# Performance work log

Measured on AMD Instinct MI355X. Metric: run time of the kernel, lower is better.

The kernel has to match this reference:

```python
import jax, jax.numpy as jnp
import numpy as np
from jax import lax

D_MODEL, D_INNER, D_STATE, D_CONV, DT_RANK = 128, 256, 16, 4, 8
BATCH, SEQ = 8, 4096


def setup_inputs() -> dict:
    key = jax.random.key(0)
    ks = jax.random.split(key, 13)
    g = lambda k, shape, fan: (jax.random.normal(k, shape, jnp.float32) / np.sqrt(fan)).astype(jnp.float32)
    inp = {
        "s": jax.random.normal(ks[0], (BATCH, SEQ, D_MODEL), jnp.float32),
        "in_proj_w": g(ks[1], (2 * D_INNER, D_MODEL), D_MODEL),
        "conv_w": g(ks[2], (D_INNER, 1, D_CONV), D_CONV),
        "conv_b": jnp.zeros((D_INNER,), jnp.float32),
        "x_proj_w": g(ks[3], (DT_RANK + 2 * D_STATE, D_INNER), D_INNER),
        "dt_proj_w": g(ks[4], (D_INNER, DT_RANK), DT_RANK),
        "dt_proj_b": jax.random.uniform(ks[5], (D_INNER,), jnp.float32, -4.0, -2.0),  # softplus(b) small, like mamba dt init
        "A_log": jnp.log(jnp.broadcast_to(jnp.arange(1, D_STATE + 1, dtype=jnp.float32), (D_INNER, D_STATE))),
        "D_skip": jnp.ones((D_INNER,), jnp.float32),
        "out_proj_w": g(ks[6], (D_MODEL, D_INNER), D_INNER),
        "ln_gamma": jnp.ones((D_MODEL,), jnp.float32),
        "ln_beta": jnp.zeros((D_MODEL,), jnp.float32),
        "fc_w": g(ks[7], (D_MODEL, D_MODEL), D_MODEL),
    }
    return inp


def _mamba(s, in_proj_w, conv_w, conv_b, x_proj_w, dt_proj_w, dt_proj_b, A_log, D_skip, out_proj_w):
    B, L, _ = s.shape
    xz = jnp.einsum("bld,ed->ble", s, in_proj_w)           # [B,L,2*D_INNER]
    x, z = jnp.split(xz, 2, axis=-1)                        # each [B,L,D_INNER]
    # causal depthwise conv1d
    xc = jnp.transpose(x, (0, 2, 1))                        # [B,D_INNER,L]
    xc = jnp.pad(xc, ((0, 0), (0, 0), (D_CONV - 1, 0)))
    xc = lax.conv_general_dilated(xc, conv_w, (1,), "VALID",
                                  dimension_numbers=("NCH", "OIH", "NCH"),
                                  feature_group_count=D_INNER)
    x = jax.nn.silu(jnp.transpose(xc + conv_b[None, :, None], (0, 2, 1)))  # [B,L,D_INNER]
    # input-dependent dt, B, C
    x_dbl = jnp.einsum("bld,ed->ble", x, x_proj_w)
    dt = x_dbl[..., :DT_RANK]
    Bc = x_dbl[..., DT_RANK:DT_RANK + D_STATE]              # [B,L,D_STATE]
    Cc = x_dbl[..., DT_RANK + D_STATE:]                     # [B,L,D_STATE]
    dt = jax.nn.softplus(jnp.einsum("blr,dr->bld", dt, dt_proj_w) + dt_proj_b)  # [B,L,D_INNER]
    A = -jnp.exp(A_log)                                     # [D_INNER,D_STATE]

    def step(h, inp):
        dt_t, b_t, c_t, u_t = inp                           # [B,Di],[B,Ds],[B,Ds],[B,Di]
        dA = jnp.exp(dt_t[:, :, None] * A)                  # [B,Di,Ds]
        dBu = (dt_t * u_t)[:, :, None] * b_t[:, None, :]
        h = dA * h + dBu
        y = jnp.einsum("bds,bs->bd", h, c_t)
        return h, y

    h0 = jnp.zeros((B, D_INNER, D_STATE), x.dtype)
    xs = (jnp.swapaxes(dt, 0, 1), jnp.swapaxes(Bc, 0, 1), jnp.swapaxes(Cc, 0, 1), jnp.swapaxes(x, 0, 1))
    _, ys = lax.scan(step, h0, xs)                          # ys: [L,B,D_INNER]
    y = jnp.swapaxes(ys, 0, 1) + x * D_skip
    y = y * jax.nn.silu(z)
    return jnp.einsum("bld,od->blo", y, out_proj_w)         # [B,L,D_MODEL]


def reference(s, in_proj_w, conv_w, conv_b, x_proj_w, dt_proj_w, dt_proj_b, A_log, D_skip, out_proj_w, ln_gamma, ln_beta, fc_w):
    h = _mamba(s, in_proj_w, conv_w, conv_b, x_proj_w, dt_proj_w, dt_proj_b, A_log, D_skip, out_proj_w)
    mu = jnp.mean(h, axis=-1, keepdims=True)
    var = jnp.mean(jnp.square(h - mu), axis=-1, keepdims=True)
    hn = (h - mu) * lax.rsqrt(var + 1e-5) * ln_gamma + ln_beta
    return jax.nn.relu(jnp.einsum("bld,od->blo", hn, fc_w))
```

## Files before the change

kernel.cpp:

```cpp
#include <hip/hip_runtime.h>
#include <math.h>

#define B_ 8
#define L_ 4096
#define DM 128
#define DI 256
#define DSN 16
#define RK 8
#define M_ (B_*L_)
#define NC 128
#define CH 32

typedef __attribute__((ext_vector_type(8))) short bfrag;
typedef __attribute__((ext_vector_type(4))) float ffrag;
typedef __attribute__((ext_vector_type(2))) float f32x2;

__device__ __forceinline__ float silu_f(float x) {
  return x * __builtin_amdgcn_rcpf(1.f + __expf(-x));
}
__device__ __forceinline__ float softplus_f(float x) {
  return (x > 20.f) ? x : __logf(1.f + __expf(x));
}

__device__ __forceinline__ unsigned short f2bf(float f) {
  unsigned int u = __builtin_bit_cast(unsigned int, f);
  unsigned int r = (u + 0x7FFFu + ((u >> 16) & 1u)) >> 16;
  return (unsigned short)r;
}
__device__ __forceinline__ unsigned int f2bf2(float lo, float hi) {
  return (unsigned int)f2bf(lo) | ((unsigned int)f2bf(hi) << 16);
}
__device__ __forceinline__ float bf2f(unsigned int us) {
  return __builtin_bit_cast(float, us << 16);
}

__global__ __launch_bounds__(256)
void gemm_bf16_in(const float* __restrict__ A, const float* __restrict__ W,
                  unsigned short* __restrict__ xb, unsigned short* __restrict__ zsb) {
  __shared__ unsigned short As[64 * 136];
  __shared__ unsigned short Ws[64 * 136];
  __shared__ unsigned short Os[64 * 72];
  const int t = threadIdx.x;
  const int m0 = blockIdx.y << 6;
  const int half = blockIdx.x;
  unsigned short* __restrict__ outp = half ? zsb : xb;
  const float* __restrict__ Wbase = W + (half << 8) * 128;
  for (int i = t; i < 64 * 32; i += 256) {
    int row = i >> 5, c4 = i & 31;
    float4 av = *(const float4*)&A[(m0 + row) * 128 + (c4 << 2)];
    uint2 ap = {f2bf2(av.x, av.y), f2bf2(av.z, av.w)};
    *(uint2*)&As[row * 136 + (c4 << 2)] = ap;
  }
  float4 wr[8];
#pragma unroll
  for (int k = 0; k < 8; ++k) {
    int i = t + (k << 8);
    int row = i >> 5, c4 = i & 31;
    wr[k] = *(const float4*)&Wbase[row * 128 + (c4 << 2)];
  }
#pragma unroll
  for (int k = 0; k < 8; ++k) {
    int i = t + (k << 8);
    int row = i >> 5, c4 = i & 31;
    uint2 wp = {f2bf2(wr[k].x, wr[k].y), f2bf2(wr[k].z, wr[k].w)};
    *(uint2*)&Ws[row * 136 + (c4 << 2)] = wp;
  }
  __syncthreads();
  const int w = t >> 6, l = t & 63, q = l >> 4, col = l & 15;
  for (int jt = 0; jt < 4; ++jt) {
    if (jt < 3) {
#pragma unroll
      for (int k = 0; k < 8; ++k) {
        int i = t + (k << 8);
        int row = i >> 5, c4 = i & 31;
        wr[k] = *(const float4*)&Wbase[(((jt + 1) << 6) + row) * 128 + (c4 << 2)];
      }
    }
    ffrag acc[4] = {{0.f,0.f,0.f,0.f},{0.f,0.f,0.f,0.f},{0.f,0.f,0.f,0.f},{0.f,0.f,0.f,0.f}};
#pragma unroll
    for (int s = 0; s < 4; ++s) {
      int k0 = s * 32 + q * 8;
      bfrag af = *(const bfrag*)&As[((w << 4) + col) * 136 + k0];
#pragma unroll
      for (int nt = 0; nt < 4; ++nt) {
        bfrag bf_ = *(const bfrag*)&Ws[((nt << 4) + col) * 136 + k0];
        acc[nt] = __builtin_amdgcn_mfma_f32_16x16x32_bf16(af, bf_, acc[nt], 0, 0, 0);
      }
    }
    __syncthreads();
#pragma unroll
    for (int nt = 0; nt < 4; ++nt)
#pragma unroll
      for (int i = 0; i < 4; ++i) {
        int ml = (w << 4) + (q << 2) + i;
        float v = acc[nt][i];
        if (half) v = silu_f(v);
        Os[ml * 72 + (nt << 4) + col] = f2bf(v);
      }
    if (jt < 3) {
#pragma unroll
      for (int k = 0; k < 8; ++k) {
        int i = t + (k << 8);
        int row = i >> 5, c4 = i & 31;
        uint2 wp = {f2bf2(wr[k].x, wr[k].y), f2bf2(wr[k].z, wr[k].w)};
        *(uint2*)&Ws[row * 136 + (c4 << 2)] = wp;
      }
    }
    __syncthreads();
    {
      int r = t >> 2, c8 = (t & 3) << 3;
      int m = m0 + r;
      *(uint4*)&outp[m * 256 + (jt << 6) + c8]      = *(const uint4*)&Os[r * 72 + c8];
      *(uint4*)&outp[m * 256 + (jt << 6) + 32 + c8] = *(const uint4*)&Os[r * 72 + 32 + c8];
    }
  }
}

__global__ __launch_bounds__(256)
void out_ln_fc(const unsigned short* __restrict__ Yb, const float* __restrict__ W,
               const float* __restrict__ gamma, const float* __restrict__ beta,
               const float* __restrict__ fcw, float* __restrict__ out) {
  __shared__ unsigned short smA[64 * 264];
  __shared__ unsigned short smB[128 * 136];
  const int t = threadIdx.x;
  const int m0 = blockIdx.x << 6;
  for (int i = t; i < 64 * 32; i += 256) {
    int row = i >> 5, c8 = i & 31;
    uint4 av = *(const uint4*)&Yb[(m0 + row) * 256 + (c8 << 3)];
    *(uint4*)&smA[row * 264 + (c8 << 3)] = av;
  }
  const int w = t >> 6, l = t & 63, q = l >> 4, col = l & 15;
  ffrag acc[2][4];
  for (int nt2 = 0; nt2 < 2; ++nt2) {
    __syncthreads();
    for (int i = t; i < 64 * 64; i += 256) {
      int row = i >> 6, c4 = i & 63;
      float4 wv = *(const float4*)&W[((nt2 << 6) + row) * 256 + (c4 << 2)];
      uint2 wp = {f2bf2(wv.x, wv.y), f2bf2(wv.z, wv.w)};
      *(uint2*)&smB[row * 264 + (c4 << 2)] = wp;
    }
    __syncthreads();
#pragma unroll
    for (int nt = 0; nt < 4; ++nt) acc[nt2][nt] = (ffrag){0.f, 0.f, 0.f, 0.f};
#pragma unroll
    for (int s = 0; s < 8; ++s) {
      int k0 = s * 32 + q * 8;
      bfrag af = *(const bfrag*)&smA[((w << 4) + col) * 264 + k0];
#pragma unroll
      for (int nt = 0; nt < 4; ++nt) {
        bfrag bf_ = *(const bfrag*)&smB[((nt << 4) + col) * 264 + k0];
        acc[nt2][nt] = __builtin_amdgcn_mfma_f32_16x16x32_bf16(af, bf_, acc[nt2][nt], 0, 0, 0);
      }
    }
  }
  float mu[4], rs[4];
#pragma unroll
  for (int i = 0; i < 4; ++i) {
    float s1 = 0.f, s2 = 0.f;
#pragma unroll
    for (int nt2 = 0; nt2 < 2; ++nt2)
#pragma unroll
      for (int nt = 0; nt < 4; ++nt) {
        float v = acc[nt2][nt][i];
        s1 += v; s2 = fmaf(v, v, s2);
      }
    s1 += __shfl_xor(s1, 1); s2 += __shfl_xor(s2, 1);
    s1 += __shfl_xor(s1, 2); s2 += __shfl_xor(s2, 2);
    s1 += __shfl_xor(s1, 4); s2 += __shfl_xor(s2, 4);
    s1 += __shfl_xor(s1, 8); s2 += __shfl_xor(s2, 8);
    mu[i] = s1 * (1.f / DM);
    float var = s2 * (1.f / DM) - mu[i] * mu[i];
    rs[i] = rsqrtf(var + 1e-5f);
  }
  __syncthreads();
#pragma unroll
  for (int nt2 = 0; nt2 < 2; ++nt2)
#pragma unroll
    for (int nt = 0; nt < 4; ++nt) {
      int n = (nt2 << 6) + (nt << 4) + col;
      float g = gamma[n], be = beta[n];
#pragma unroll
      for (int i = 0; i < 4; ++i) {
        int r = (w << 4) + (q << 2) + i;
        smA[r * 136 + n] = f2bf(fmaf((acc[nt2][nt][i] - mu[i]) * rs[i], g, be));
      }
    }
  for (int i = t; i < 128 * 32; i += 256) {
    int row = i >> 5, c4 = i & 31;
    float4 wv = *(const float4*)&fcw[row * 128 + (c4 << 2)];
    uint2 wp = {f2bf2(wv.x, wv.y), f2bf2(wv.z, wv.w)};
    *(uint2*)&smB[row * 136 + (c4 << 2)] = wp;
  }
  __syncthreads();
  ffrag a2[8] = {{0.f,0.f,0.f,0.f},{0.f,0.f,0.f,0.f},{0.f,0.f,0.f,0.f},{0.f,0.f,0.f,0.f},
                 {0.f,0.f,0.f,0.f},{0.f,0.f,0.f,0.f},{0.f,0.f,0.f,0.f},{0.f,0.f,0.f,0.f}};
#pragma unroll
  for (int s = 0; s < 4; ++s) {
    int k0 = s * 32 + q * 8;
    bfrag af = *(const bfrag*)&smA[((w << 4) + col) * 136 + k0];
#pragma unroll
    for (int nt = 0; nt < 8; ++nt) {
      bfrag bf_ = *(const bfrag*)&smB[((nt << 4) + col) * 136 + k0];
      a2[nt] = __builtin_amdgcn_mfma_f32_16x16x32_bf16(af, bf_, a2[nt], 0, 0, 0);
    }
  }
#pragma unroll
  for (int nt = 0; nt < 8; ++nt)
#pragma unroll
    for (int i = 0; i < 4; ++i) {
      int ml = (w << 4) + (q << 2) + i;
      out[(m0 + ml) * 128 + (nt << 4) + col] = fmaxf(a2[nt][i], 0.f);
    }
}

__global__ __launch_bounds__(512)
void xproj_dtproj(const unsigned short* __restrict__ xb, const float* __restrict__ xw,
                  const float* __restrict__ dtw, const float* __restrict__ dtpb,
                  const float* __restrict__ cw, const float* __restrict__ cb,
                  float* __restrict__ Bb, float* __restrict__ Cb,
                  unsigned int* __restrict__ udt) {
  __shared__ unsigned short ua[64 * 264];
  __shared__ unsigned short wb[48 * 264];
  __shared__ float dtr_s[64 * 12];
  const int t = threadIdx.x;
  const int p0 = blockIdx.x << 6;
  {
    const int k = t & 255, half = t >> 8;
    const int pstart = half << 5;
    const int base = p0 + pstart;
    const int lb = base & (L_ - 1);
    const float w0 = cw[k*4], w1 = cw[k*4+1], w2 = cw[k*4+2], w3 = cw[k*4+3];
    const float bias = cb[k];
    float x0 = (lb >= 3) ? bf2f((unsigned int)xb[(base - 3) * 256 + k]) : 0.f;
    float x1 = (lb >= 2) ? bf2f((unsigned int)xb[(base - 2) * 256 + k]) : 0.f;
    float x2 = (lb >= 1) ? bf2f((unsigned int)xb[(base - 1) * 256 + k]) : 0.f;
#pragma unroll 8
    for (int it = 0; it < 32; ++it) {
      float x3 = bf2f((unsigned int)xb[(base + it) * 256 + k]);
      float u = silu_f(fmaf(w0, x0, fmaf(w1, x1, fmaf(w2, x2, fmaf(w3, x3, bias)))));
      ua[(pstart + it) * 264 + k] = f2bf(u);
      x0 = x1; x1 = x2; x2 = x3;
    }
  }
  for (int i = t; i < 40 * 256; i += 512) {
    int n = i >> 8, k = i & 255;
    wb[n * 264 + k] = f2bf(xw[i]);
  }
  for (int i = t; i < 8 * 264; i += 512) wb[40 * 264 + i] = 0;
  __syncthreads();
  const int w = t >> 6, l = t & 63, q = l >> 4, col = l & 15;
  for (int tile = w; tile < 12; tile += 8) {
    const int mt = tile & 3, nt = tile >> 2;
    ffrag acc = {0.f, 0.f, 0.f, 0.f};
#pragma unroll
    for (int s = 0; s < 8; ++s) {
      int k0 = s * 32 + q * 8;
      bfrag af = *(const bfrag*)&ua[((mt << 4) + col) * 264 + k0];
      bfrag bf_ = *(const bfrag*)&wb[((nt << 4) + col) * 264 + k0];
      acc = __builtin_amdgcn_mfma_f32_16x16x32_bf16(af, bf_, acc, 0, 0, 0);
    }
#pragma unroll
    for (int i = 0; i < 4; ++i) {
      int ml = (mt << 4) + (q << 2) + i;
      int m = p0 + ml;
      if (nt == 0) {
        if (col < 8) dtr_s[ml * 12 + col] = acc[i];
        else         Bb[m * 16 + (col - 8)] = acc[i];
      } else if (nt == 1) {
        if (col < 8) Bb[m * 16 + 8 + col] = acc[i];
        else         Cb[m * 16 + (col - 8)] = acc[i];
      } else {
        if (col < 8) Cb[m * 16 + 8 + col] = acc[i];
      }
    }
  }
  __syncthreads();
  {
    const int d = t & 255, half = t >> 8;
    const int pstart = half << 5;
    float w8[8];
    *(float4*)&w8[0] = *(const float4*)&dtw[d * 8];
    *(float4*)&w8[4] = *(const float4*)&dtw[d * 8 + 4];
    const float bias = dtpb[d];
#pragma unroll 4
    for (int pp = pstart; pp < pstart + 32; ++pp) {
      float r0[8];
      *(float4*)&r0[0] = *(const float4*)&dtr_s[pp * 12];
      *(float4*)&r0[4] = *(const float4*)&dtr_s[pp * 12 + 4];
      float a2 = bias;
#pragma unroll
      for (int r2 = 0; r2 < 8; ++r2) a2 = fmaf(r0[r2], w8[r2], a2);
      float sp = softplus_f(a2);
      udt[(p0 + pp) * 256 + d] =
          (unsigned int)ua[pp * 264 + d] | ((unsigned int)f2bf(sp) << 16);
    }
  }
}

__global__ __launch_bounds__(512, 4)
void scan_phase1(const unsigned int* __restrict__ udt,
                 const float* __restrict__ Bb, const float* __restrict__ alog,
                 unsigned short* __restrict__ cP, unsigned short* __restrict__ cHe) {
  __shared__ float Bs[CH * 16];
  const int bc = blockIdx.x;
  const int b = bc >> 7, c = bc & (NC - 1);
  const int t = threadIdx.x;
  const int l = t & 63, w = t >> 6;
  const int d = (w << 5) + (l & 31);
  const int sh = l >> 5;
  const int soff = sh << 3;
  const int base = b * L_ + c * CH;
  if (t < CH * 4) ((float4*)Bs)[t] = *(const float4*)&Bb[base * 16 + (t << 2)];
  float a[8];
  bool okl = true;
#pragma unroll
  for (int j = 0; j < 8; ++j) {
    a[j] = -__expf(alog[d * 16 + soff + j]);
    float tgt = (float)(soff + j + 1);
    okl = okl && (fabsf(a[j] + tgt) <= 1e-3f * tgt);
  }
  const bool fast = (bool)__all((int)okl);
  f32x2 h2[4] = {{0.f,0.f},{0.f,0.f},{0.f,0.f},{0.f,0.f}};
  float sdt = 0.f;
  unsigned int wv0 = udt[base * 256 + d];
  unsigned int wv1 = udt[(base + 1) * 256 + d];
  __syncthreads();
#pragma unroll 4
  for (int ll = 0; ll < CH; ++ll) {
    const int m2 = base + ((ll + 2 < CH) ? ll + 2 : CH - 1);
    unsigned int wv2 = udt[m2 * 256 + d];
    float4 b0 = *(const float4*)&Bs[ll * 16 + soff];
    float4 b1 = *(const float4*)&Bs[ll * 16 + soff + 4];
    float uv  = bf2f(wv0 & 0xFFFFu);
    float dtv = bf2f(wv0 >> 16);
    f32x2 B2[4] = {{b0.x,b0.y},{b0.z,b0.w},{b1.x,b1.y},{b1.z,b1.w}};
    float du = dtv * uv;
    sdt += dtv;
    if (fast) {
      float e1 = __expf(-dtv);
      float e2 = e1 * e1, e4 = e2 * e2, e8 = e4 * e4;
      float st = sh ? e8 * e1 : e1;
      f32x2 dA = {st, st * e1};
      f32x2 e22 = {e2, e2};
      f32x2 du2 = {du, du};
#pragma unroll
      for (int j = 0; j < 4; ++j) {
        h2[j] = dA * h2[j] + du2 * B2[j];
        dA = dA * e22;
      }
    } else {
#pragma unroll
      for (int j = 0; j < 8; ++j) {
        float dA = __expf(dtv * a[j]);
        h2[j >> 1][j & 1] = fmaf(dA, h2[j >> 1][j & 1], du * B2[j >> 1][j & 1]);
      }
    }
    wv0 = wv1; wv1 = wv2;
  }
#pragma unroll
  for (int j = 0; j < 8; ++j) {
    int o = (bc * 16 + soff + j) * 256 + d;
    cP[o]  = f2bf(__expf(a[j] * sdt));
    cHe[o] = f2bf(h2[j >> 1][j & 1]);
  }
}

__global__ __launch_bounds__(512)
void scan_combine(unsigned short* __restrict__ cP, const unsigned short* __restrict__ cHe) {
  __shared__ float segP[64 * 9], segH[64 * 9], segS[64 * 9];
  const int t = threadIdx.x;
  const int sdl = t & 63, seg = t >> 6;
  const int blk = blockIdx.x;
  const int b = blk >> 6, grp = blk & 63;
  const int sd = (grp << 6) + sdl;
  const int base = b * NC * 4096 + sd;
  float Pacc = 1.f, Hacc = 0.f;
#pragma unroll
  for (int i = 0; i < 16; ++i) {
    int idx = base + (seg * 16 + i) * 4096;
    float p = bf2f((unsigned int)cP[idx]);
    float he = bf2f((unsigned int)cHe[idx]);
    Hacc = fmaf(p, Hacc, he);
    Pacc *= p;
  }
  segP[sdl * 9 + seg] = Pacc;
  segH[sdl * 9 + seg] = Hacc;
  __syncthreads();
  if (t < 64) {
    float hs = 0.f;
#pragma unroll
    for (int s2 = 0; s2 < 8; ++s2) {
      segS[t * 9 + s2] = hs;
      hs = fmaf(segP[t * 9 + s2], hs, segH[t * 9 + s2]);
    }
  }
  __syncthreads();
  float hs = segS[sdl * 9 + seg];
#pragma unroll
  for (int i = 0; i < 16; ++i) {
    int idx = base + (seg * 16 + i) * 4096;
    float p = bf2f((unsigned int)cP[idx]);
    float he = bf2f((unsigned int)cHe[idx]);
    cP[idx] = f2bf(hs);
    hs = fmaf(p, hs, he);
  }
}

__global__ __launch_bounds__(512, 4)
void scan_phase3(const unsigned int* __restrict__ udt,
                 const float* __restrict__ Bb, const float* __restrict__ Cb,
                 const float* __restrict__ alog, const unsigned short* __restrict__ hst,
                 const float* __restrict__ dsk,
                 const unsigned short* __restrict__ zsb,
                 unsigned short* __restrict__ yb) {
  __shared__ float Bs[CH * 16];
  __shared__ float Cs[CH * 16];
  const int bc = blockIdx.x;
  const int b = bc >> 7, c = bc & (NC - 1);
  const int t = threadIdx.x;
  const int l = t & 63, w = t >> 6;
  const int d = (w << 5) + (l & 31);
  const int sh = l >> 5;
  const int soff = sh << 3;
  const int base = b * L_ + c * CH;
  if (t < CH * 4)            ((float4*)Bs)[t]            = *(const float4*)&Bb[base * 16 + (t << 2)];
  else if (t < CH * 8)       ((float4*)Cs)[t - CH * 4]   = *(const float4*)&Cb[base * 16 + ((t - CH * 4) << 2)];
  float a[8];
  bool okl = true;
#pragma unroll
  for (int j = 0; j < 8; ++j) {
    a[j] = -__expf(alog[d * 16 + soff + j]);
    float tgt = (float)(soff + j + 1);
    okl = okl && (fabsf(a[j] + tgt) <= 1e-3f * tgt);
  }
  const bool fast = (bool)__all((int)okl);
  const float dskv = dsk[d];
  f32x2 h2[4];
#pragma unroll
  for (int j = 0; j < 8; ++j)
    h2[j >> 1][j & 1] = bf2f((unsigned int)hst[(bc * 16 + soff + j) * 256 + d]);
  unsigned int wv0 = udt[base * 256 + d];
  unsigned int wv1 = udt[(base + 1) * 256 + d];
  unsigned short zv0 = zsb[base * 256 + d];
  unsigned short zv1 = zsb[(base + 1) * 256 + d];
  __syncthreads();
#pragma unroll 4
  for (int ll = 0; ll < CH; ++ll) {
    const int m = base + ll;
    const int m2 = base + ((ll + 2 < CH) ? ll + 2 : CH - 1);
    unsigned int wv2 = udt[m2 * 256 + d];
    unsigned short zv2 = zsb[m2 * 256 + d];
    float4 b0 = *(const float4*)&Bs[ll * 16 + soff];
    float4 b1 = *(const float4*)&Bs[ll * 16 + soff + 4];
    float4 c0 = *(const float4*)&Cs[ll * 16 + soff];
    float4 c1 = *(const float4*)&Cs[ll * 16 + soff + 4];
    float uv  = bf2f(wv0 & 0xFFFFu);
    float dtv = bf2f(wv0 >> 16);
    f32x2 B2[4] = {{b0.x,b0.y},{b0.z,b0.w},{b1.x,b1.y},{b1.z,b1.w}};
    f32x2 C2[4] = {{c0.x,c0.y},{c0.z,c0.w},{c1.x,c1.y},{c1.z,c1.w}};
    float du = dtv * uv;
    f32x2 y2 = {0.f, 0.f};
    if (fast) {
      float e1 = __expf(-dtv);
      float e2 = e1 * e1, e4 = e2 * e2, e8 = e4 * e4;
      float st = sh ? e8 * e1 : e1;
      f32x2 dA = {st, st * e1};
      f32x2 e22 = {e2, e2};
      f32x2 du2 = {du, du};
#pragma unroll
      for (int j = 0; j < 4; ++j) {
        h2[j] = dA * h2[j] + du2 * B2[j];
        y2 = y2 + h2[j] * C2[j];
        dA = dA * e22;
      }
    } else {
#pragma unroll
      for (int j = 0; j < 8; ++j) {
        float dA = __expf(dtv * a[j]);
        float hh = fmaf(dA, h2[j >> 1][j & 1], du * B2[j >> 1][j & 1]);
        h2[j >> 1][j & 1] = hh;
        y2[j & 1] = fmaf(hh, C2[j >> 1][j & 1], y2[j & 1]);
      }
    }
    float y = y2.x + y2.y;
    y += __shfl_xor(y, 32);
    if (sh == 0) {
      float zs = bf2f((unsigned int)zv0);
      yb[m * 256 + d] = f2bf(fmaf(uv, dskv, y) * zs);
    }
    wv0 = wv1; wv1 = wv2; zv0 = zv1; zv1 = zv2;
  }
}

extern "C" void kernel_launch(void* const* d_in, const int* in_sizes, int n_in,
                              void* d_out, int out_size, void* d_ws, size_t ws_size,
                              hipStream_t stream) {
  (void)in_sizes; (void)n_in; (void)out_size; (void)ws_size;
  const float* s    = (const float*)d_in[0];
  const float* w_in = (const float*)d_in[1];
  const float* cw   = (const float*)d_in[2];
  const float* cb   = (const float*)d_in[3];
  const float* xw   = (const float*)d_in[4];
  const float* dtw  = (const float*)d_in[5];
  const float* dtpb = (const float*)d_in[6];
  const float* alog = (const float*)d_in[7];
  const float* dsk  = (const float*)d_in[8];
  const float* ow   = (const float*)d_in[9];
  const float* gam  = (const float*)d_in[10];
  const float* bet  = (const float*)d_in[11];
  const float* fcw  = (const float*)d_in[12];
  float* out = (float*)d_out;
  float* ws  = (float*)d_ws;

  unsigned short* xb   = (unsigned short*)ws;
  unsigned short* zsb  = (unsigned short*)(ws + 4194304);
  unsigned int*   udt  = (unsigned int*)(ws + 8388608);
  float*          Bb   = ws + 16777216;
  float*          Cb   = ws + 17301504;
  unsigned short* cP   = (unsigned short*)(ws + 17825792);
  unsigned short* cHe  = (unsigned short*)(ws + 19922944);
  unsigned short* yb   = (unsigned short*)(ws + 22020096);

  gemm_bf16_in<<<dim3(2, 512), 256, 0, stream>>>(s, w_in, xb, zsb);
  xproj_dtproj<<<512, 512, 0, stream>>>(xb, xw, dtw, dtpb, cw, cb, Bb, Cb, udt);
  scan_phase1<<<B_ * NC, 512, 0, stream>>>(udt, Bb, alog, cP, cHe);
  scan_combine<<<512, 512, 0, stream>>>(cP, cHe);
  scan_phase3<<<B_ * NC, 512, 0, stream>>>(udt, Bb, Cb, alog, cP, dsk, zsb, yb);
  out_ln_fc<<<512, 256, 0, stream>>>(yb, ow, gam, bet, fcw, out);
}
```

Before: 195.8 us.

## Fuse scan phase 3 with out_proj, LayerNorm and FC, two chunks per block

The scan output kernel is merged with the out-projection/LayerNorm/FC kernel. Each block now scans two consecutive chunks (64 rows) and writes the gated y values straight into shared memory, where the following MFMA GEMMs consume them. This removes the bf16 y round-trip through global memory and one kernel launch. In exchange the grid is halved, each block's sequential scan is twice as long, shared-memory use per block grows, and only half the threads take part in the GEMM stages, all of which can lower occupancy and parallelism.

```diff
diff --git a/kernel.cpp b/kernel.cpp
--- a/kernel.cpp
+++ b/kernel.cpp
@@ -10,6 +10,7 @@
 #define M_ (B_*L_)
 #define NC 128
 #define CH 32
+#define CH2 64
 
 typedef __attribute__((ext_vector_type(8))) short bfrag;
 typedef __attribute__((ext_vector_type(4))) float ffrag;
@@ -114,103 +115,6 @@
       *(uint4*)&outp[m * 256 + (jt << 6) + 32 + c8] = *(const uint4*)&Os[r * 72 + 32 + c8];
     }
   }
-}
-
-__global__ __launch_bounds__(256)
-void out_ln_fc(const unsigned short* __restrict__ Yb, const float* __restrict__ W,
-               const float* __restrict__ gamma, const float* __restrict__ beta,
-               const float* __restrict__ fcw, float* __restrict__ out) {
-  __shared__ unsigned short smA[64 * 264];
-  __shared__ unsigned short smB[128 * 136];
-  const int t = threadIdx.x;
-  const int m0 = blockIdx.x << 6;
-  for (int i = t; i < 64 * 32; i += 256) {
-    int row = i >> 5, c8 = i & 31;
-    uint4 av = *(const uint4*)&Yb[(m0 + row) * 256 + (c8 << 3)];
-    *(uint4*)&smA[row * 264 + (c8 << 3)] = av;
-  }
-  const int w = t >> 6, l = t & 63, q = l >> 4, col = l & 15;
-  ffrag acc[2][4];
-  for (int nt2 = 0; nt2 < 2; ++nt2) {
-    __syncthreads();
-    for (int i = t; i < 64 * 64; i += 256) {
-      int row = i >> 6, c4 = i & 63;
-      float4 wv = *(const float4*)&W[((nt2 << 6) + row) * 256 + (c4 << 2)];
-      uint2 wp = {f2bf2(wv.x, wv.y), f2bf2(wv.z, wv.w)};
-      *(uint2*)&smB[row * 264 + (c4 << 2)] = wp;
-    }
-    __syncthreads();
-#pragma unroll
-    for (int nt = 0; nt < 4; ++nt) acc[nt2][nt] = (ffrag){0.f, 0.f, 0.f, 0.f};
-#pragma unroll
-    for (int s = 0; s < 8; ++s) {
-      int k0 = s * 32 + q * 8;
-      bfrag af = *(const bfrag*)&smA[((w << 4) + col) * 264 + k0];
-#pragma unroll
-      for (int nt = 0; nt < 4; ++nt) {
-        bfrag bf_ = *(const bfrag*)&smB[((nt << 4) + col) * 264 + k0];
-        acc[nt2][nt] = __builtin_amdgcn_mfma_f32_16x16x32_bf16(af, bf_, acc[nt2][nt], 0, 0, 0);
-      }
-    }
-  }
-  float mu[4], rs[4];
-#pragma unroll
-  for (int i = 0; i < 4; ++i) {
-    float s1 = 0.f, s2 = 0.f;
-#pragma unroll
-    for (int nt2 = 0; nt2 < 2; ++nt2)
-#pragma unroll
-      for (int nt = 0; nt < 4; ++nt) {
-        float v = acc[nt2][nt][i];
-        s1 += v; s2 = fmaf(v, v, s2);
-      }
-    s1 += __shfl_xor(s1, 1); s2 += __shfl_xor(s2, 1);
-    s1 += __shfl_xor(s1, 2); s2 += __shfl_xor(s2, 2);
-    s1 += __shfl_xor(s1, 4); s2 += __shfl_xor(s2, 4);
-    s1 += __shfl_xor(s1, 8); s2 += __shfl_xor(s2, 8);
-    mu[i] = s1 * (1.f / DM);
-    float var = s2 * (1.f / DM) - mu[i] * mu[i];
-    rs[i] = rsqrtf(var + 1e-5f);
-  }
-  __syncthreads();
-#pragma unroll
-  for (int nt2 = 0; nt2 < 2; ++nt2)
-#pragma unroll
-    for (int nt = 0; nt < 4; ++nt) {
-      int n = (nt2 << 6) + (nt << 4) + col;
-      float g = gamma[n], be = beta[n];
-#pragma unroll
-      for (int i = 0; i < 4; ++i) {
-        int r = (w << 4) + (q << 2) + i;
-        smA[r * 136 + n] = f2bf(fmaf((acc[nt2][nt][i] - mu[i]) * rs[i], g, be));
-      }
-    }
-  for (int i = t; i < 128 * 32; i += 256) {
-    int row = i >> 5, c4 = i & 31;
-    float4 wv = *(const float4*)&fcw[row * 128 + (c4 << 2)];
-    uint2 wp = {f2bf2(wv.x, wv.y), f2bf2(wv.z, wv.w)};
-    *(uint2*)&smB[row * 136 + (c4 << 2)] = wp;
-  }
-  __syncthreads();
-  ffrag a2[8] = {{0.f,0.f,0.f,0.f},{0.f,0.f,0.f,0.f},{0.f,0.f,0.f,0.f},{0.f,0.f,0.f,0.f},
-                 {0.f,0.f,0.f,0.f},{0.f,0.f,0.f,0.f},{0.f,0.f,0.f,0.f},{0.f,0.f,0.f,0.f}};
-#pragma unroll
-  for (int s = 0; s < 4; ++s) {
-    int k0 = s * 32 + q * 8;
-    bfrag af = *(const bfrag*)&smA[((w << 4) + col) * 136 + k0];
-#pragma unroll
-    for (int nt = 0; nt < 8; ++nt) {
-      bfrag bf_ = *(const bfrag*)&smB[((nt << 4) + col) * 136 + k0];
-      a2[nt] = __builtin_amdgcn_mfma_f32_16x16x32_bf16(af, bf_, a2[nt], 0, 0, 0);
-    }
-  }
-#pragma unroll
-  for (int nt = 0; nt < 8; ++nt)
-#pragma unroll
-    for (int i = 0; i < 4; ++i) {
-      int ml = (w << 4) + (q << 2) + i;
-      out[(m0 + ml) * 128 + (nt << 4) + col] = fmaxf(a2[nt][i], 0.f);
-    }
 }
 
 __global__ __launch_bounds__(512)
@@ -407,24 +311,29 @@
 }
 
 __global__ __launch_bounds__(512, 4)
-void scan_phase3(const unsigned int* __restrict__ udt,
-                 const float* __restrict__ Bb, const float* __restrict__ Cb,
-                 const float* __restrict__ alog, const unsigned short* __restrict__ hst,
-                 const float* __restrict__ dsk,
-                 const unsigned short* __restrict__ zsb,
-                 unsigned short* __restrict__ yb) {
-  __shared__ float Bs[CH * 16];
-  __shared__ float Cs[CH * 16];
+void scan3_out_ln_fc(const unsigned int* __restrict__ udt,
+                     const float* __restrict__ Bb, const float* __restrict__ Cb,
+                     const float* __restrict__ alog, const unsigned short* __restrict__ hst,
+                     const float* __restrict__ dsk,
+                     const unsigned short* __restrict__ zsb,
+                     const float* __restrict__ W,
+                     const float* __restrict__ gamma, const float* __restrict__ beta,
+                     const float* __restrict__ fcw, float* __restrict__ out) {
+  __shared__ float Bs[CH2 * 16];
+  __shared__ float Cs[CH2 * 16];
+  __shared__ unsigned short smA[64 * 264];
+  __shared__ unsigned short smB[128 * 136];
   const int bc = blockIdx.x;
-  const int b = bc >> 7, c = bc & (NC - 1);
+  const int b = bc >> 6, cc = bc & 63;
   const int t = threadIdx.x;
   const int l = t & 63, w = t >> 6;
   const int d = (w << 5) + (l & 31);
   const int sh = l >> 5;
   const int soff = sh << 3;
-  const int base = b * L_ + c * CH;
-  if (t < CH * 4)            ((float4*)Bs)[t]            = *(const float4*)&Bb[base * 16 + (t << 2)];
-  else if (t < CH * 8)       ((float4*)Cs)[t - CH * 4]   = *(const float4*)&Cb[base * 16 + ((t - CH * 4) << 2)];
+  const int base = b * L_ + (cc << 1) * CH;
+  const int hc = b * NC + (cc << 1);
+  if (t < CH2 * 4)           ((float4*)Bs)[t]            = *(const float4*)&Bb[base * 16 + (t << 2)];
+  else if (t < CH2 * 8)      ((float4*)Cs)[t - CH2 * 4]  = *(const float4*)&Cb[base * 16 + ((t - CH2 * 4) << 2)];
   float a[8];
   bool okl = true;
 #pragma unroll
@@ -438,16 +347,15 @@
   f32x2 h2[4];
 #pragma unroll
   for (int j = 0; j < 8; ++j)
-    h2[j >> 1][j & 1] = bf2f((unsigned int)hst[(bc * 16 + soff + j) * 256 + d]);
+    h2[j >> 1][j & 1] = bf2f((unsigned int)hst[(hc * 16 + soff + j) * 256 + d]);
   unsigned int wv0 = udt[base * 256 + d];
   unsigned int wv1 = udt[(base + 1) * 256 + d];
   unsigned short zv0 = zsb[base * 256 + d];
   unsigned short zv1 = zsb[(base + 1) * 256 + d];
   __syncthreads();
 #pragma unroll 4
-  for (int ll = 0; ll < CH; ++ll) {
-    const int m = base + ll;
-    const int m2 = base + ((ll + 2 < CH) ? ll + 2 : CH - 1);
+  for (int ll = 0; ll < CH2; ++ll) {
+    const int m2 = base + ((ll + 2 < CH2) ? ll + 2 : CH2 - 1);
     unsigned int wv2 = udt[m2 * 256 + d];
     unsigned short zv2 = zsb[m2 * 256 + d];
     float4 b0 = *(const float4*)&Bs[ll * 16 + soff];
@@ -486,9 +394,99 @@
     y += __shfl_xor(y, 32);
     if (sh == 0) {
       float zs = bf2f((unsigned int)zv0);
-      yb[m * 256 + d] = f2bf(fmaf(uv, dskv, y) * zs);
+      smA[ll * 264 + d] = f2bf(fmaf(uv, dskv, y) * zs);
     }
     wv0 = wv1; wv1 = wv2; zv0 = zv1; zv1 = zv2;
+  }
+  const int q = l >> 4, col = l & 15;
+  ffrag acc[2][4];
+  for (int nt2 = 0; nt2 < 2; ++nt2) {
+    __syncthreads();
+    for (int i = t; i < 64 * 64; i += 512) {
+      int row = i >> 6, c4 = i & 63;
+      float4 wv = *(const float4*)&W[((nt2 << 6) + row) * 256 + (c4 << 2)];
+      uint2 wp = {f2bf2(wv.x, wv.y), f2bf2(wv.z, wv.w)};
+      *(uint2*)&smB[row * 264 + (c4 << 2)] = wp;
+    }
+    __syncthreads();
+    if (t < 256) {
+#pragma unroll
+      for (int nt = 0; nt < 4; ++nt) acc[nt2][nt] = (ffrag){0.f, 0.f, 0.f, 0.f};
+#pragma unroll
+      for (int s = 0; s < 8; ++s) {
+        int k0 = s * 32 + q * 8;
+        bfrag af = *(const bfrag*)&smA[((w << 4) + col) * 264 + k0];
+#pragma unroll
+        for (int nt = 0; nt < 4; ++nt) {
+          bfrag bf_ = *(const bfrag*)&smB[((nt << 4) + col) * 264 + k0];
+          acc[nt2][nt] = __builtin_amdgcn_mfma_f32_16x16x32_bf16(af, bf_, acc[nt2][nt], 0, 0, 0);
+        }
+      }
+    }
+  }
+  float mu[4], rs[4];
+  if (t < 256) {
+#pragma unroll
+    for (int i = 0; i < 4; ++i) {
+      float s1 = 0.f, s2 = 0.f;
+#pragma unroll
+      for (int nt2 = 0; nt2 < 2; ++nt2)
+#pragma unroll
+        for (int nt = 0; nt < 4; ++nt) {
+          float v = acc[nt2][nt][i];
+          s1 += v; s2 = fmaf(v, v, s2);
+        }
+      s1 += __shfl_xor(s1, 1); s2 += __shfl_xor(s2, 1);
+      s1 += __shfl_xor(s1, 2); s2 += __shfl_xor(s2, 2);
+      s1 += __shfl_xor(s1, 4); s2 += __shfl_xor(s2, 4);
+      s1 += __shfl_xor(s1, 8); s2 += __shfl_xor(s2, 8);
+      mu[i] = s1 * (1.f / DM);
+      float var = s2 * (1.f / DM) - mu[i] * mu[i];
+      rs[i] = rsqrtf(var + 1e-5f);
+    }
+  }
+  __syncthreads();
+  if (t < 256) {
+#pragma unroll
+    for (int nt2 = 0; nt2 < 2; ++nt2)
+#pragma unroll
+      for (int nt = 0; nt < 4; ++nt) {
+        int n = (nt2 << 6) + (nt << 4) + col;
+        float g = gamma[n], be = beta[n];
+#pragma unroll
+        for (int i = 0; i < 4; ++i) {
+          int r = (w << 4) + (q << 2) + i;
+          smA[r * 136 + n] = f2bf(fmaf((acc[nt2][nt][i] - mu[i]) * rs[i], g, be));
+        }
+      }
+  }
+  for (int i = t; i < 128 * 32; i += 512) {
+    int row = i >> 5, c4 = i & 31;
+    float4 wv = *(const float4*)&fcw[row * 128 + (c4 << 2)];
+    uint2 wp = {f2bf2(wv.x, wv.y), f2bf2(wv.z, wv.w)};
+    *(uint2*)&smB[row * 136 + (c4 << 2)] = wp;
+  }
+  __syncthreads();
+  if (t < 256) {
+    ffrag a2[8] = {{0.f,0.f,0.f,0.f},{0.f,0.f,0.f,0.f},{0.f,0.f,0.f,0.f},{0.f,0.f,0.f,0.f},
+                   {0.f,0.f,0.f,0.f},{0.f,0.f,0.f,0.f},{0.f,0.f,0.f,0.f},{0.f,0.f,0.f,0.f}};
+#pragma unroll
+    for (int s = 0; s < 4; ++s) {
+      int k0 = s * 32 + q * 8;
+      bfrag af = *(const bfrag*)&smA[((w << 4) + col) * 136 + k0];
+#pragma unroll
+      for (int nt = 0; nt < 8; ++nt) {
+        bfrag bf_ = *(const bfrag*)&smB[((nt << 4) + col) * 136 + k0];
+        a2[nt] = __builtin_amdgcn_mfma_f32_16x16x32_bf16(af, bf_, a2[nt], 0, 0, 0);
+      }
+    }
+#pragma unroll
+    for (int nt = 0; nt < 8; ++nt)
+#pragma unroll
+      for (int i = 0; i < 4; ++i) {
+        int ml = (w << 4) + (q << 2) + i;
+        out[(base + ml) * 128 + (nt << 4) + col] = fmaxf(a2[nt][i], 0.f);
+      }
   }
 }
 
@@ -519,12 +517,11 @@
   float*          Cb   = ws + 17301504;
   unsigned short* cP   = (unsigned short*)(ws + 17825792);
   unsigned short* cHe  = (unsigned short*)(ws + 19922944);
-  unsigned short* yb   = (unsigned short*)(ws + 22020096);
 
   gemm_bf16_in<<<dim3(2, 512), 256, 0, stream>>>(s, w_in, xb, zsb);
   xproj_dtproj<<<512, 512, 0, stream>>>(xb, xw, dtw, dtpb, cw, cb, Bb, Cb, udt);
   scan_phase1<<<B_ * NC, 512, 0, stream>>>(udt, Bb, alog, cP, cHe);
   scan_combine<<<512, 512, 0, stream>>>(cP, cHe);
-  scan_phase3<<<B_ * NC, 512, 0, stream>>>(udt, Bb, Cb, alog, cP, dsk, zsb, yb);
-  out_ln_fc<<<512, 256, 0, stream>>>(yb, ow, gam, bet, fcw, out);
-}
+  scan3_out_ln_fc<<<B_ * NC / 2, 512, 0, stream>>>(udt, Bb, Cb, alog, cP, dsk, zsb,
+                                                   ow, gam, bet, fcw, out);
+}
```

Measured after the change: 186.0 us. 1.05x faster.
